# Kernel optimization log

Hardware: AMD Instinct MI355X
Metric: run time of the kernel (lower is better)

Reference implementation:

```python
import jax, jax.numpy as jnp
import numpy as np

N = 50000      # nodes
E = 800000     # edges
DIN = 128      # in_channels
H = 128        # hidden_channels
G = 64         # graphs in batch
OUT = 8        # head out_channels


def setup_inputs() -> dict:
    key = jax.random.key(0)
    ks = jax.random.split(key, 12)
    s = 0.1  # weight init scale
    x = jax.random.normal(ks[0], (N, DIN), jnp.float32)
    edge_index = jax.random.randint(ks[1], (2, E), 0, N, dtype=jnp.int64)
    batch = jnp.sort(jax.random.randint(ks[2], (N,), 0, G, dtype=jnp.int64))
    W0 = jax.random.normal(ks[3], (DIN, H), jnp.float32) * s
    b0 = jnp.zeros((H,), jnp.float32)
    W1 = jax.random.normal(ks[4], (H, H), jnp.float32) * s
    b1 = jnp.zeros((H,), jnp.float32)
    W2 = jax.random.normal(ks[5], (H, H), jnp.float32) * s
    b2 = jnp.zeros((H,), jnp.float32)
    Wh = jax.random.normal(ks[6], (H, OUT), jnp.float32) * s
    bh = jnp.zeros((OUT,), jnp.float32)
    return {"x": x, "edge_index": edge_index, "batch": batch,
            "W0": W0, "b0": b0, "W1": W1, "b1": b1, "W2": W2, "b2": b2,
            "Wh": Wh, "bh": bh}


def gcn_conv(x, src, dst, W, b):
    # GCNConv with self-loops and symmetric normalization (PyG defaults).
    h = x @ W                                           # [N, H]
    deg = jnp.zeros((N,), h.dtype).at[dst].add(1.0) + 1.0   # in-degree incl. self-loop
    dinv = jax.lax.rsqrt(deg)                           # deg^{-1/2}
    coef = dinv[src] * dinv[dst]                        # [E]
    agg = jnp.zeros_like(h).at[dst].add(h[src] * coef[:, None])
    # self-loop contribution: dinv[i]^2 * h[i]
    return agg + h * (dinv * dinv)[:, None] + b


def reference(x, edge_index, batch, W0, b0, W1, b1, W2, b2, Wh, bh):
    src, dst = edge_index[0], edge_index[1]
    h = jax.nn.relu(gcn_conv(x, src, dst, W0, b0))
    h = jax.nn.relu(gcn_conv(h, src, dst, W1, b1))
    h = gcn_conv(h, src, dst, W2, b2)                   # last layer: no activation
    # global mean pool over graphs
    sums = jnp.zeros((G, H), h.dtype).at[batch].add(h)
    cnt = jnp.zeros((G,), h.dtype).at[batch].add(1.0)
    pooled = sums / jnp.maximum(cnt, 1.0)[:, None]      # [G, H]
    return pooled @ Wh + bh                             # [G, OUT]
```

## Files before the change

### kernel.cpp

```cpp
#include <hip/hip_runtime.h>

#define N_NODES 50000
#define N_EDGES 800000
#define HD 128
#define NGRAPH 64
#define NOUT 8
#define SLOTS 64
#define MMGRID 782
#define GAGRID 3125

typedef __attribute__((ext_vector_type(8))) short bf8_t;
typedef __attribute__((ext_vector_type(4))) float f4_t;
typedef __attribute__((ext_vector_type(8))) unsigned short us8;

__device__ __forceinline__ unsigned short f2b(float f) {
    unsigned u = __float_as_uint(f);
    u += 0x7fffu + ((u >> 16) & 1u);
    return (unsigned short)(u >> 16);
}
__device__ __forceinline__ float b2f(unsigned short h) {
    return __uint_as_float(((unsigned)h) << 16);
}

__global__ __launch_bounds__(256) void cvtw_k(const float* __restrict__ W0,
                                              const float* __restrict__ W1,
                                              const float* __restrict__ W2,
                                              unsigned short* __restrict__ WT) {
    int idx = blockIdx.x * 256 + threadIdx.x;
    if (idx >= 3 * HD * HD) return;
    int w = idx >> 14;
    int rem = idx & 16383;
    int n = rem >> 7;
    int k = rem & 127;
    const float* W = (w == 0) ? W0 : (w == 1) ? W1 : W2;
    WT[(size_t)w * HD * HD + n * HD + k] = f2b(W[k * HD + n]);
}

__global__ __launch_bounds__(256) void fillmm_k(const float* __restrict__ X,
                                                const unsigned short* __restrict__ WT,
                                                const int* __restrict__ src,
                                                const int* __restrict__ dst,
                                                int* __restrict__ degc,
                                                unsigned short* __restrict__ slots,
                                                unsigned short* __restrict__ Y) {
    if (blockIdx.x < MMGRID) {
        const int lane = threadIdx.x & 63;
        const int wave = threadIdx.x >> 6;
        const int r = lane & 15;
        const int q = lane >> 4;
        const int row0 = blockIdx.x * 64 + wave * 16;
        int arow = row0 + r; if (arow >= N_NODES) arow = N_NODES - 1;

        f4_t acc[8];
#pragma unroll
        for (int n = 0; n < 8; ++n) acc[n] = (f4_t){0.f, 0.f, 0.f, 0.f};

#pragma unroll
        for (int kb = 0; kb < 4; ++kb) {
            float4 fa = *(const float4*)(X + (size_t)arow * HD + kb * 32 + q * 8);
            float4 fb = *(const float4*)(X + (size_t)arow * HD + kb * 32 + q * 8 + 4);
            bf8_t a;
            a[0] = (short)f2b(fa.x); a[1] = (short)f2b(fa.y);
            a[2] = (short)f2b(fa.z); a[3] = (short)f2b(fa.w);
            a[4] = (short)f2b(fb.x); a[5] = (short)f2b(fb.y);
            a[6] = (short)f2b(fb.z); a[7] = (short)f2b(fb.w);
#pragma unroll
            for (int n = 0; n < 8; ++n) {
                bf8_t b = *(const bf8_t*)(WT + (size_t)(n * 16 + r) * HD + kb * 32 + q * 8);
                acc[n] = __builtin_amdgcn_mfma_f32_16x16x32_bf16(a, b, acc[n], 0, 0, 0);
            }
        }
        const int orow = row0 + q * 4;
#pragma unroll
        for (int i = 0; i < 4; ++i) {
            int rr = orow + i;
            if (rr < N_NODES) {
#pragma unroll
                for (int n = 0; n < 8; ++n)
                    Y[(size_t)rr * HD + n * 16 + r] = f2b(acc[n][i]);
            }
        }
        return;
    }
    int e = (blockIdx.x - MMGRID) * 256 + threadIdx.x;
    if (e >= N_EDGES) return;
    int s = __builtin_nontemporal_load(src + e);
    int d = __builtin_nontemporal_load(dst + e);
    int pos = atomicAdd(&degc[d], 1);
    if (pos < SLOTS)
        slots[(size_t)d * SLOTS + pos] = (unsigned short)s;
}

__global__ __launch_bounds__(256) void fusedGM2c_k(const unsigned short* __restrict__ T,
                                                   const int* __restrict__ degc,
                                                   const unsigned short* __restrict__ slots,
                                                   const float* __restrict__ bias,
                                                   const unsigned short* __restrict__ WT,
                                                   unsigned short* __restrict__ Y) {
    __shared__ unsigned short hs[16][136];
    const int tid = threadIdx.x;
    const int base = blockIdx.x * 16;

    {
        const int g = tid >> 4;
        const int l = tid & 15;
        const int j8 = l * 8;
        const int i = base + g;
        const int dg = degc[i];
        int dc = dg; if (dc > SLOTS) dc = SLOTS;
        const float di = rsqrtf((float)dg + 1.0f);
        const unsigned short* sl = slots + (size_t)i * SLOTS;

        float a[8];
#pragma unroll
        for (int k = 0; k < 8; ++k) a[k] = 0.f;
        int e = 0;
        for (; e + 15 < dc; e += 16) {
            us8 i0 = *(const us8*)(sl + e);
            us8 i1 = *(const us8*)(sl + e + 8);
            float c[16];
#pragma unroll
            for (int u = 0; u < 8; ++u) c[u]     = rsqrtf((float)degc[i0[u]] + 1.0f);
#pragma unroll
            for (int u = 0; u < 8; ++u) c[u + 8] = rsqrtf((float)degc[i1[u]] + 1.0f);
            us8 v[16];
#pragma unroll
            for (int u = 0; u < 8; ++u) v[u]     = *(const us8*)(T + (size_t)i0[u] * HD + j8);
#pragma unroll
            for (int u = 0; u < 8; ++u) v[u + 8] = *(const us8*)(T + (size_t)i1[u] * HD + j8);
#pragma unroll
            for (int u = 0; u < 16; ++u) {
#pragma unroll
                for (int k = 0; k < 8; ++k) a[k] = fmaf(c[u], b2f(v[u][k]), a[k]);
            }
        }
        if (e < dc) {
            us8 i0 = *(const us8*)(sl + e);
            us8 i1 = *(const us8*)(sl + e + 8);
            const unsigned short safe = i0[0];
            int s[16]; float mc[16];
#pragma unroll
            for (int u = 0; u < 8; ++u) {
                bool ok = (e + u < dc);
                s[u] = ok ? i0[u] : safe;
                mc[u] = ok ? rsqrtf((float)degc[s[u]] + 1.0f) : 0.f;
            }
#pragma unroll
            for (int u = 0; u < 8; ++u) {
                bool ok = (e + 8 + u < dc);
                s[u + 8] = ok ? i1[u] : safe;
                mc[u + 8] = ok ? rsqrtf((float)degc[s[u + 8]] + 1.0f) : 0.f;
            }
            us8 v[16];
#pragma unroll
            for (int u = 0; u < 16; ++u) v[u] = *(const us8*)(T + (size_t)s[u] * HD + j8);
#pragma unroll
            for (int u = 0; u < 16; ++u) {
#pragma unroll
                for (int k = 0; k < 8; ++k) a[k] = fmaf(mc[u], b2f(v[u][k]), a[k]);
            }
        }
        us8 tv = *(const us8*)(T + (size_t)i * HD + j8);
        float4 bv0 = *(const float4*)(bias + j8);
        float4 bv1 = *(const float4*)(bias + j8 + 4);
        float bb[8] = {bv0.x, bv0.y, bv0.z, bv0.w, bv1.x, bv1.y, bv1.z, bv1.w};
        us8 o;
#pragma unroll
        for (int k = 0; k < 8; ++k) {
            float r = di * (a[k] + di * b2f(tv[k])) + bb[k];
            r = fmaxf(r, 0.f);
            o[k] = f2b(r);
        }
        *(us8*)(&hs[g][j8]) = o;
    }
    __syncthreads();

    {
        const int lane = tid & 63;
        const int wave = tid >> 6;
        const int r = lane & 15;
        const int q = lane >> 4;
        const int n0 = wave * 2;

        f4_t acc0 = (f4_t){0.f, 0.f, 0.f, 0.f};
        f4_t acc1 = (f4_t){0.f, 0.f, 0.f, 0.f};
#pragma unroll
        for (int kb = 0; kb < 4; ++kb) {
            bf8_t a = *(const bf8_t*)(&hs[r][kb * 32 + q * 8]);
            bf8_t b0 = *(const bf8_t*)(WT + (size_t)(n0 * 16 + r) * HD + kb * 32 + q * 8);
            bf8_t b1 = *(const bf8_t*)(WT + (size_t)(n0 * 16 + 16 + r) * HD + kb * 32 + q * 8);
            acc0 = __builtin_amdgcn_mfma_f32_16x16x32_bf16(a, b0, acc0, 0, 0, 0);
            acc1 = __builtin_amdgcn_mfma_f32_16x16x32_bf16(a, b1, acc1, 0, 0, 0);
        }
#pragma unroll
        for (int i = 0; i < 4; ++i) {
            int rr = base + q * 4 + i;
            float dv = rsqrtf((float)degc[rr] + 1.0f);
            Y[(size_t)rr * HD + n0 * 16 + r]      = f2b(acc0[i] * dv);
            Y[(size_t)rr * HD + n0 * 16 + 16 + r] = f2b(acc1[i] * dv);
        }
    }
}

__global__ __launch_bounds__(256) void fusedGM2_k(const unsigned short* __restrict__ T,
                                                  const int* __restrict__ degc,
                                                  const unsigned short* __restrict__ slots,
                                                  const float* __restrict__ bias,
                                                  const unsigned short* __restrict__ WT,
                                                  unsigned short* __restrict__ Y) {
    __shared__ unsigned short hs[16][136];
    const int tid = threadIdx.x;
    const int base = blockIdx.x * 16;

    {
        const int g = tid >> 4;
        const int l = tid & 15;
        const int j8 = l * 8;
        const int i = base + g;
        const int dg = degc[i];
        int dc = dg; if (dc > SLOTS) dc = SLOTS;
        const float di = rsqrtf((float)dg + 1.0f);
        const unsigned short* sl = slots + (size_t)i * SLOTS;

        float a[8];
#pragma unroll
        for (int k = 0; k < 8; ++k) a[k] = 0.f;
        int e = 0;
        for (; e + 15 < dc; e += 16) {
            us8 i0 = *(const us8*)(sl + e);
            us8 i1 = *(const us8*)(sl + e + 8);
            us8 v[16];
#pragma unroll
            for (int u = 0; u < 8; ++u) v[u]     = *(const us8*)(T + (size_t)i0[u] * HD + j8);
#pragma unroll
            for (int u = 0; u < 8; ++u) v[u + 8] = *(const us8*)(T + (size_t)i1[u] * HD + j8);
#pragma unroll
            for (int u = 0; u < 16; ++u) {
#pragma unroll
                for (int k = 0; k < 8; ++k) a[k] += b2f(v[u][k]);
            }
        }
        if (e < dc) {
            us8 i0 = *(const us8*)(sl + e);
            us8 i1 = *(const us8*)(sl + e + 8);
            const unsigned short safe = i0[0];
            int s[16]; float m[16];
#pragma unroll
            for (int u = 0; u < 8; ++u) {
                m[u] = (e + u < dc) ? 1.f : 0.f;
                s[u] = (e + u < dc) ? i0[u] : safe;
            }
#pragma unroll
            for (int u = 0; u < 8; ++u) {
                m[u + 8] = (e + 8 + u < dc) ? 1.f : 0.f;
                s[u + 8] = (e + 8 + u < dc) ? i1[u] : safe;
            }
            us8 v[16];
#pragma unroll
            for (int u = 0; u < 16; ++u) v[u] = *(const us8*)(T + (size_t)s[u] * HD + j8);
#pragma unroll
            for (int u = 0; u < 16; ++u) {
#pragma unroll
                for (int k = 0; k < 8; ++k) a[k] = fmaf(m[u], b2f(v[u][k]), a[k]);
            }
        }
        us8 tv = *(const us8*)(T + (size_t)i * HD + j8);
        float4 bv0 = *(const float4*)(bias + j8);
        float4 bv1 = *(const float4*)(bias + j8 + 4);
        float bb[8] = {bv0.x, bv0.y, bv0.z, bv0.w, bv1.x, bv1.y, bv1.z, bv1.w};
        us8 o;
#pragma unroll
        for (int k = 0; k < 8; ++k) {
            float r = di * (a[k] + b2f(tv[k])) + bb[k];
            r = fmaxf(r, 0.f);
            o[k] = f2b(r);
        }
        *(us8*)(&hs[g][j8]) = o;
    }
    __syncthreads();

    {
        const int lane = tid & 63;
        const int wave = tid >> 6;
        const int r = lane & 15;
        const int q = lane >> 4;
        const int n0 = wave * 2;

        f4_t acc0 = (f4_t){0.f, 0.f, 0.f, 0.f};
        f4_t acc1 = (f4_t){0.f, 0.f, 0.f, 0.f};
#pragma unroll
        for (int kb = 0; kb < 4; ++kb) {
            bf8_t a = *(const bf8_t*)(&hs[r][kb * 32 + q * 8]);
            bf8_t b0 = *(const bf8_t*)(WT + (size_t)(n0 * 16 + r) * HD + kb * 32 + q * 8);
            bf8_t b1 = *(const bf8_t*)(WT + (size_t)(n0 * 16 + 16 + r) * HD + kb * 32 + q * 8);
            acc0 = __builtin_amdgcn_mfma_f32_16x16x32_bf16(a, b0, acc0, 0, 0, 0);
            acc1 = __builtin_amdgcn_mfma_f32_16x16x32_bf16(a, b1, acc1, 0, 0, 0);
        }
#pragma unroll
        for (int i = 0; i < 4; ++i) {
            int rr = base + q * 4 + i;
            float dv = rsqrtf((float)degc[rr] + 1.0f);
            Y[(size_t)rr * HD + n0 * 16 + r]      = f2b(acc0[i] * dv);
            Y[(size_t)rr * HD + n0 * 16 + 16 + r] = f2b(acc1[i] * dv);
        }
    }
}

__global__ __launch_bounds__(256) void gpool_k(const unsigned short* __restrict__ T,
                                               const int* __restrict__ degc,
                                               const unsigned short* __restrict__ slots,
                                               const float* __restrict__ b,
                                               const int* __restrict__ batch,
                                               float* __restrict__ sums,
                                               float* __restrict__ cnt) {
    __shared__ float hsf[16][128];
    const int tid = threadIdx.x;
    const int base = blockIdx.x * 16;

    {
        const int g = tid >> 4;
        const int j8 = (tid & 15) * 8;
        const int i = base + g;
        const int dg = degc[i];
        int dc = dg; if (dc > SLOTS) dc = SLOTS;
        const float di = rsqrtf((float)dg + 1.0f);
        const unsigned short* sl = slots + (size_t)i * SLOTS;

        float a[8];
#pragma unroll
        for (int k = 0; k < 8; ++k) a[k] = 0.f;
        int e = 0;
        for (; e + 15 < dc; e += 16) {
            us8 i0 = *(const us8*)(sl + e);
            us8 i1 = *(const us8*)(sl + e + 8);
            us8 v[16];
#pragma unroll
            for (int u = 0; u < 8; ++u) v[u]     = *(const us8*)(T + (size_t)i0[u] * HD + j8);
#pragma unroll
            for (int u = 0; u < 8; ++u) v[u + 8] = *(const us8*)(T + (size_t)i1[u] * HD + j8);
#pragma unroll
            for (int u = 0; u < 16; ++u) {
#pragma unroll
                for (int k = 0; k < 8; ++k) a[k] += b2f(v[u][k]);
            }
        }
        if (e < dc) {
            us8 i0 = *(const us8*)(sl + e);
            us8 i1 = *(const us8*)(sl + e + 8);
            const unsigned short safe = i0[0];
            int s[16]; float m[16];
#pragma unroll
            for (int u = 0; u < 8; ++u) {
                m[u] = (e + u < dc) ? 1.f : 0.f;
                s[u] = (e + u < dc) ? i0[u] : safe;
            }
#pragma unroll
            for (int u = 0; u < 8; ++u) {
                m[u + 8] = (e + 8 + u < dc) ? 1.f : 0.f;
                s[u + 8] = (e + 8 + u < dc) ? i1[u] : safe;
            }
            us8 v[16];
#pragma unroll
            for (int u = 0; u < 16; ++u) v[u] = *(const us8*)(T + (size_t)s[u] * HD + j8);
#pragma unroll
            for (int u = 0; u < 16; ++u) {
#pragma unroll
                for (int k = 0; k < 8; ++k) a[k] = fmaf(m[u], b2f(v[u][k]), a[k]);
            }
        }
        us8 tv = *(const us8*)(T + (size_t)i * HD + j8);
        float4 bv0 = *(const float4*)(b + j8);
        float4 bv1 = *(const float4*)(b + j8 + 4);
        float bb[8] = {bv0.x, bv0.y, bv0.z, bv0.w, bv1.x, bv1.y, bv1.z, bv1.w};
#pragma unroll
        for (int k = 0; k < 8; ++k)
            hsf[g][j8 + k] = di * (a[k] + b2f(tv[k])) + bb[k];
    }
    __syncthreads();

    {
        const int f = tid & 127;
        const int half = tid >> 7;
        const int r0 = half * 8;
        int cur = batch[base + r0];
        float acc = 0.f;
        float c = 0.f;
#pragma unroll
        for (int r = r0; r < r0 + 8; ++r) {
            int gg = batch[base + r];
            if (gg != cur) {
                atomicAdd(&sums[cur * HD + f], acc);
                if (f == 0) atomicAdd(&cnt[cur], c);
                acc = 0.f; c = 0.f; cur = gg;
            }
            acc += hsf[r][f];
            c += 1.f;
        }
        atomicAdd(&sums[cur * HD + f], acc);
        if (f == 0) atomicAdd(&cnt[cur], c);
    }
}

__global__ __launch_bounds__(512) void head_k(const float* __restrict__ sums,
                                              const float* __restrict__ cnt,
                                              const float* __restrict__ Wh,
                                              const float* __restrict__ bh,
                                              float* __restrict__ out) {
    int t = threadIdx.x;
    int g = t >> 3, o = t & 7;
    float inv = 1.0f / fmaxf(cnt[g], 1.0f);
    float acc = bh[o];
    for (int h = 0; h < HD; ++h)
        acc += sums[g * HD + h] * inv * Wh[h * NOUT + o];
    out[g * NOUT + o] = acc;
}

extern "C" void kernel_launch(void* const* d_in, const int* in_sizes, int n_in,
                              void* d_out, int out_size, void* d_ws, size_t ws_size,
                              hipStream_t stream) {
    const float* x  = (const float*)d_in[0];
    const int*   ei = (const int*)d_in[1];
    const int*   batch = (const int*)d_in[2];
    const float* W0 = (const float*)d_in[3];
    const float* b0 = (const float*)d_in[4];
    const float* W1 = (const float*)d_in[5];
    const float* b1 = (const float*)d_in[6];
    const float* W2 = (const float*)d_in[7];
    const float* b2 = (const float*)d_in[8];
    const float* Wh = (const float*)d_in[9];
    const float* bh = (const float*)d_in[10];
    float* out = (float*)d_out;

    const int* src = ei;
    const int* dst = ei + N_EDGES;

    char* wsb = (char*)d_ws;
    int*            degc  = (int*)(wsb + 0);
    unsigned short* slots = (unsigned short*)(wsb + 200000);
    unsigned short* WT    = (unsigned short*)(wsb + 6600000);
    unsigned short* A     = (unsigned short*)(wsb + 6698304);
    unsigned short* C     = (unsigned short*)(wsb + 19498304);
    float*          sums  = (float*)(wsb + 32298304);
    float*          cnt   = (float*)(wsb + 32331072);

    const int fillGrid = (N_EDGES + 255) / 256;

    hipMemsetAsync(degc, 0, N_NODES * sizeof(int), stream);
    hipMemsetAsync(sums, 0, (NGRAPH * HD + NGRAPH) * sizeof(float), stream);
    cvtw_k<<<(3 * HD * HD + 255) / 256, 256, 0, stream>>>(W0, W1, W2, WT);

    fillmm_k<<<MMGRID + fillGrid, 256, 0, stream>>>(x, WT, src, dst, degc, slots, A);

    fusedGM2c_k<<<GAGRID, 256, 0, stream>>>(A, degc, slots, b0, WT + HD * HD, C);

    fusedGM2_k<<<GAGRID, 256, 0, stream>>>(C, degc, slots, b1, WT + 2 * HD * HD, A);

    gpool_k<<<GAGRID, 256, 0, stream>>>(A, degc, slots, b2, batch, sums, cnt);

    head_k<<<1, 512, 0, stream>>>(sums, cnt, Wh, bh, out);
}
```

Baseline: 347.9 us.

## Fold memsets into weight-convert kernel, interleave GEMM/fill blocks, add nontemporal hints

The two hipMemsetAsync calls are removed and the zeroing of degree counters, pooled sums and counts moves into the weight-conversion kernel, which cuts two launches. In the combined fill+matmul kernel, one block in every five now does the GEMM and the rest do edge bucketing, so both kinds of work run at the same time instead of GEMM blocks being dispatched first. Nontemporal loads and stores are also added for the X reads, slot index reads and output writes, to reduce cache pollution. This adds division and modulo arithmetic on the block index, and the nontemporal hints could hurt if those lines would otherwise be reused from cache.

```diff
diff --git a/kernel.cpp b/kernel.cpp
--- a/kernel.cpp
+++ b/kernel.cpp
@@ -6,7 +6,8 @@
 #define NGRAPH 64
 #define NOUT 8
 #define SLOTS 64
-#define MMGRID 782
+#define GEMM_GRID 782
+#define FILL_GRID 3125
 #define GAGRID 3125
 
 typedef __attribute__((ext_vector_type(8))) short bf8_t;
@@ -25,15 +26,22 @@
 __global__ __launch_bounds__(256) void cvtw_k(const float* __restrict__ W0,
                                               const float* __restrict__ W1,
                                               const float* __restrict__ W2,
-                                              unsigned short* __restrict__ WT) {
+                                              unsigned short* __restrict__ WT,
+                                              int* __restrict__ degc,
+                                              float* __restrict__ sums,
+                                              float* __restrict__ cnt) {
     int idx = blockIdx.x * 256 + threadIdx.x;
-    if (idx >= 3 * HD * HD) return;
-    int w = idx >> 14;
-    int rem = idx & 16383;
-    int n = rem >> 7;
-    int k = rem & 127;
-    const float* W = (w == 0) ? W0 : (w == 1) ? W1 : W2;
-    WT[(size_t)w * HD * HD + n * HD + k] = f2b(W[k * HD + n]);
+    if (idx < 3 * HD * HD) {
+        int w = idx >> 14;
+        int rem = idx & 16383;
+        int n = rem >> 7;
+        int k = rem & 127;
+        const float* W = (w == 0) ? W0 : (w == 1) ? W1 : W2;
+        WT[(size_t)w * HD * HD + n * HD + k] = f2b(W[k * HD + n]);
+    }
+    if (idx < N_NODES) degc[idx] = 0;
+    if (idx < NGRAPH * HD) sums[idx] = 0.f;
+    if (idx < NGRAPH) cnt[idx] = 0.f;
 }
 
 __global__ __launch_bounds__(256) void fillmm_k(const float* __restrict__ X,
@@ -43,12 +51,14 @@
                                                 int* __restrict__ degc,
                                                 unsigned short* __restrict__ slots,
                                                 unsigned short* __restrict__ Y) {
-    if (blockIdx.x < MMGRID) {
+    const unsigned b = blockIdx.x;
+    if (b % 5u == 4u) {
+        const int g = b / 5u;
         const int lane = threadIdx.x & 63;
         const int wave = threadIdx.x >> 6;
         const int r = lane & 15;
         const int q = lane >> 4;
-        const int row0 = blockIdx.x * 64 + wave * 16;
+        const int row0 = g * 64 + wave * 16;
         int arow = row0 + r; if (arow >= N_NODES) arow = N_NODES - 1;
 
         f4_t acc[8];
@@ -57,17 +67,17 @@
 
 #pragma unroll
         for (int kb = 0; kb < 4; ++kb) {
-            float4 fa = *(const float4*)(X + (size_t)arow * HD + kb * 32 + q * 8);
-            float4 fb = *(const float4*)(X + (size_t)arow * HD + kb * 32 + q * 8 + 4);
+            f4_t fa = __builtin_nontemporal_load((const f4_t*)(X + (size_t)arow * HD + kb * 32 + q * 8));
+            f4_t fb = __builtin_nontemporal_load((const f4_t*)(X + (size_t)arow * HD + kb * 32 + q * 8 + 4));
             bf8_t a;
-            a[0] = (short)f2b(fa.x); a[1] = (short)f2b(fa.y);
-            a[2] = (short)f2b(fa.z); a[3] = (short)f2b(fa.w);
-            a[4] = (short)f2b(fb.x); a[5] = (short)f2b(fb.y);
-            a[6] = (short)f2b(fb.z); a[7] = (short)f2b(fb.w);
+            a[0] = (short)f2b(fa[0]); a[1] = (short)f2b(fa[1]);
+            a[2] = (short)f2b(fa[2]); a[3] = (short)f2b(fa[3]);
+            a[4] = (short)f2b(fb[0]); a[5] = (short)f2b(fb[1]);
+            a[6] = (short)f2b(fb[2]); a[7] = (short)f2b(fb[3]);
 #pragma unroll
             for (int n = 0; n < 8; ++n) {
-                bf8_t b = *(const bf8_t*)(WT + (size_t)(n * 16 + r) * HD + kb * 32 + q * 8);
-                acc[n] = __builtin_amdgcn_mfma_f32_16x16x32_bf16(a, b, acc[n], 0, 0, 0);
+                bf8_t bb = *(const bf8_t*)(WT + (size_t)(n * 16 + r) * HD + kb * 32 + q * 8);
+                acc[n] = __builtin_amdgcn_mfma_f32_16x16x32_bf16(a, bb, acc[n], 0, 0, 0);
             }
         }
         const int orow = row0 + q * 4;
@@ -77,13 +87,14 @@
             if (rr < N_NODES) {
 #pragma unroll
                 for (int n = 0; n < 8; ++n)
-                    Y[(size_t)rr * HD + n * 16 + r] = f2b(acc[n][i]);
+                    __builtin_nontemporal_store(f2b(acc[n][i]), Y + (size_t)rr * HD + n * 16 + r);
             }
         }
         return;
     }
-    int e = (blockIdx.x - MMGRID) * 256 + threadIdx.x;
-    if (e >= N_EDGES) return;
+    const unsigned sb = b - (b + 1u) / 5u;
+    if (sb >= FILL_GRID) return;
+    int e = sb * 256 + threadIdx.x;
     int s = __builtin_nontemporal_load(src + e);
     int d = __builtin_nontemporal_load(dst + e);
     int pos = atomicAdd(&degc[d], 1);
@@ -116,8 +127,8 @@
         for (int k = 0; k < 8; ++k) a[k] = 0.f;
         int e = 0;
         for (; e + 15 < dc; e += 16) {
-            us8 i0 = *(const us8*)(sl + e);
-            us8 i1 = *(const us8*)(sl + e + 8);
+            us8 i0 = __builtin_nontemporal_load((const us8*)(sl + e));
+            us8 i1 = __builtin_nontemporal_load((const us8*)(sl + e + 8));
             float c[16];
 #pragma unroll
             for (int u = 0; u < 8; ++u) c[u]     = rsqrtf((float)degc[i0[u]] + 1.0f);
@@ -135,8 +146,8 @@
             }
         }
         if (e < dc) {
-            us8 i0 = *(const us8*)(sl + e);
-            us8 i1 = *(const us8*)(sl + e + 8);
+            us8 i0 = __builtin_nontemporal_load((const us8*)(sl + e));
+            us8 i1 = __builtin_nontemporal_load((const us8*)(sl + e + 8));
             const unsigned short safe = i0[0];
             int s[16]; float mc[16];
 #pragma unroll
@@ -196,8 +207,8 @@
         for (int i = 0; i < 4; ++i) {
             int rr = base + q * 4 + i;
             float dv = rsqrtf((float)degc[rr] + 1.0f);
-            Y[(size_t)rr * HD + n0 * 16 + r]      = f2b(acc0[i] * dv);
-            Y[(size_t)rr * HD + n0 * 16 + 16 + r] = f2b(acc1[i] * dv);
+            __builtin_nontemporal_store(f2b(acc0[i] * dv), Y + (size_t)rr * HD + n0 * 16 + r);
+            __builtin_nontemporal_store(f2b(acc1[i] * dv), Y + (size_t)rr * HD + n0 * 16 + 16 + r);
         }
     }
 }
@@ -227,8 +238,8 @@
         for (int k = 0; k < 8; ++k) a[k] = 0.f;
         int e = 0;
         for (; e + 15 < dc; e += 16) {
-            us8 i0 = *(const us8*)(sl + e);
-            us8 i1 = *(const us8*)(sl + e + 8);
+            us8 i0 = __builtin_nontemporal_load((const us8*)(sl + e));
+            us8 i1 = __builtin_nontemporal_load((const us8*)(sl + e + 8));
             us8 v[16];
 #pragma unroll
             for (int u = 0; u < 8; ++u) v[u]     = *(const us8*)(T + (size_t)i0[u] * HD + j8);
@@ -241,8 +252,8 @@
             }
         }
         if (e < dc) {
-            us8 i0 = *(const us8*)(sl + e);
-            us8 i1 = *(const us8*)(sl + e + 8);
+            us8 i0 = __builtin_nontemporal_load((const us8*)(sl + e));
+            us8 i1 = __builtin_nontemporal_load((const us8*)(sl + e + 8));
             const unsigned short safe = i0[0];
             int s[16]; float m[16];
 #pragma unroll
@@ -300,8 +311,8 @@
         for (int i = 0; i < 4; ++i) {
             int rr = base + q * 4 + i;
             float dv = rsqrtf((float)degc[rr] + 1.0f);
-            Y[(size_t)rr * HD + n0 * 16 + r]      = f2b(acc0[i] * dv);
-            Y[(size_t)rr * HD + n0 * 16 + 16 + r] = f2b(acc1[i] * dv);
+            __builtin_nontemporal_store(f2b(acc0[i] * dv), Y + (size_t)rr * HD + n0 * 16 + r);
+            __builtin_nontemporal_store(f2b(acc1[i] * dv), Y + (size_t)rr * HD + n0 * 16 + 16 + r);
         }
     }
 }
@@ -331,8 +342,8 @@
         for (int k = 0; k < 8; ++k) a[k] = 0.f;
         int e = 0;
         for (; e + 15 < dc; e += 16) {
-            us8 i0 = *(const us8*)(sl + e);
-            us8 i1 = *(const us8*)(sl + e + 8);
+            us8 i0 = __builtin_nontemporal_load((const us8*)(sl + e));
+            us8 i1 = __builtin_nontemporal_load((const us8*)(sl + e + 8));
             us8 v[16];
 #pragma unroll
             for (int u = 0; u < 8; ++u) v[u]     = *(const us8*)(T + (size_t)i0[u] * HD + j8);
@@ -345,8 +356,8 @@
             }
         }
         if (e < dc) {
-            us8 i0 = *(const us8*)(sl + e);
-            us8 i1 = *(const us8*)(sl + e + 8);
+            us8 i0 = __builtin_nontemporal_load((const us8*)(sl + e));
+            us8 i1 = __builtin_nontemporal_load((const us8*)(sl + e + 8));
             const unsigned short safe = i0[0];
             int s[16]; float m[16];
 #pragma unroll
@@ -443,13 +454,9 @@
     float*          sums  = (float*)(wsb + 32298304);
     float*          cnt   = (float*)(wsb + 32331072);
 
-    const int fillGrid = (N_EDGES + 255) / 256;
-
-    hipMemsetAsync(degc, 0, N_NODES * sizeof(int), stream);
-    hipMemsetAsync(sums, 0, (NGRAPH * HD + NGRAPH) * sizeof(float), stream);
-    cvtw_k<<<(3 * HD * HD + 255) / 256, 256, 0, stream>>>(W0, W1, W2, WT);
-
-    fillmm_k<<<MMGRID + fillGrid, 256, 0, stream>>>(x, WT, src, dst, degc, slots, A);
+    cvtw_k<<<(N_NODES + 255) / 256, 256, 0, stream>>>(W0, W1, W2, WT, degc, sums, cnt);
+
+    fillmm_k<<<3910, 256, 0, stream>>>(x, WT, src, dst, degc, slots, A);
 
     fusedGM2c_k<<<GAGRID, 256, 0, stream>>>(A, degc, slots, b0, WT + HD * HD, C);
 
```

New measurement: 337.5 us. -3.0%, faster.
